# Optimization experiments

Hardware: AMD Instinct MI355X
Metric: run time of the kernel (lower is better)

## Reference

```python
import jax, jax.numpy as jnp
import numpy as np

DIM = 2048
NH = 16
HD = DIM // NH  # 128


def setup_inputs() -> dict:
    key = jax.random.key(0)
    ks = jax.random.split(key, 9)
    s_in = 1.0 / np.sqrt(DIM)
    inp = {
        "x": jax.random.normal(ks[0], (2, 2048, DIM), dtype=jnp.float32),
        # torch Linear weights stored as (out, in); we keep (in, out) for x @ W
        "wq": jax.random.uniform(ks[1], (DIM, DIM), jnp.float32, -s_in, s_in),
        "bq": jax.random.uniform(ks[2], (DIM,), jnp.float32, -s_in, s_in),
        "wk": jax.random.uniform(ks[3], (DIM, HD), jnp.float32, -s_in, s_in),
        "bk": jax.random.uniform(ks[4], (HD,), jnp.float32, -s_in, s_in),
        "wv": jax.random.uniform(ks[5], (DIM, HD), jnp.float32, -s_in, s_in),
        "bv": jax.random.uniform(ks[6], (HD,), jnp.float32, -s_in, s_in),
        "wo": jax.random.uniform(ks[7], (DIM, DIM), jnp.float32, -s_in, s_in),
        "bo": jax.random.uniform(ks[8], (DIM,), jnp.float32, -s_in, s_in),
    }
    return inp


def reference(x, wq, bq, wk, bk, wv, bv, wo, bo):
    bs, sl, dim = x.shape
    q = x @ wq + bq                      # [b, s, dim]
    k = x @ wk + bk                      # [b, s, hd] (single shared KV head)
    v = x @ wv + bv                      # [b, s, hd]
    q = q.reshape(bs, sl, NH, HD)        # [b, s, h, hd]
    scale = 1.0 / np.sqrt(HD).astype(np.float32)
    # scores: broadcast single KV head over all query heads
    attn = jnp.einsum('bshd,btd->bhst', q, k) * scale   # [b, h, s, s]
    att = jax.nn.softmax(attn, axis=-1)
    o = jnp.einsum('bhst,btd->bshd', att, v)            # [b, s, h, hd]
    o = o.reshape(bs, sl, dim)
    return o @ wo + bo
```

## Files before the change

kernel.cpp:

```cpp
#include <hip/hip_runtime.h>
#include <hip/hip_bf16.h>
#include <math.h>

#define DIM 2048
#define NH 16
#define HD 128
#define BATCH 2
#define SEQ 2048
#define TOKENS (BATCH * SEQ)
#define NQKV (DIM + 2 * HD)

typedef __attribute__((ext_vector_type(8))) _Float16 f16x8;
typedef __attribute__((ext_vector_type(4))) float f32x4;
typedef unsigned short u16;
typedef unsigned int u32;

typedef union { u32 d[4]; f16x8 v; } frag_u;

__device__ __forceinline__ u16 f2h(float f) {
    union { _Float16 h; u16 u; } v; v.h = (_Float16)f; return v.u;
}
__device__ __forceinline__ void gll16(const void* g, void* l) {
    __builtin_amdgcn_global_load_lds(
        (const __attribute__((address_space(1))) unsigned int*)g,
        (__attribute__((address_space(3))) unsigned int*)l, 16, 0, 0);
}

#define KIDX(r, c) ((r) * 128 + (((((c) << 1)) ^ (((r) & 7) << 4)) >> 1))
#define VIDX(d, c) ((d) * 64  + (((((c) << 1)) ^ (((d) & 7) << 4)) >> 1))

__global__ __launch_bounds__(256) void conv_f16(
    const float* __restrict__ in, u16* __restrict__ out)
{
    const int i = blockIdx.x * 256 + threadIdx.x;
    const float4 v = ((const float4*)in)[i];
    ushort4 h;
    h.x = f2h(v.x); h.y = f2h(v.y); h.z = f2h(v.z); h.w = f2h(v.w);
    ((ushort4*)out)[i] = h;
}

__global__ __launch_bounds__(256) void transpose_f16(
    const float* __restrict__ W, u16* __restrict__ T, int K, int N, int rowoff)
{
    __shared__ float tile[32][33];
    const int k0 = blockIdx.x * 32;
    const int n0 = blockIdx.y * 32;
    const int tid = threadIdx.x;
#pragma unroll
    for (int i = 0; i < 4; ++i) {
        const int idx = tid + i * 256;
        const int r = idx >> 5, c = idx & 31;
        tile[r][c] = W[(size_t)(k0 + r) * N + n0 + c];
    }
    __syncthreads();
#pragma unroll
    for (int i = 0; i < 4; ++i) {
        const int idx = tid + i * 256;
        const int r = idx >> 5, c = idx & 31;
        T[(size_t)(rowoff + n0 + r) * K + k0 + c] = f2h(tile[c][r]);
    }
}

__global__ __launch_bounds__(256) void concat_bias(
    const float* __restrict__ bq, const float* __restrict__ bk,
    const float* __restrict__ bv, float* __restrict__ bc)
{
    const int i = blockIdx.x * 256 + threadIdx.x;
    float v;
    if (i < DIM) v = bq[i];
    else if (i < DIM + HD) v = bk[i - DIM];
    else v = bv[i - DIM - HD];
    bc[i] = v;
}

template <int MODE>
__global__ __launch_bounds__(256) void gemm_f16(
    const u16* __restrict__ A, const u16* __restrict__ B,
    const float* __restrict__ bias, float* __restrict__ Cf,
    u16* __restrict__ qdst, u16* __restrict__ kdst, u16* __restrict__ vtdst,
    float scale)
{
    constexpr int BK = 32;
    __shared__ u16 lds[2][2 * 128 * BK];

    const int tid = threadIdx.x;
    const int wid = tid >> 6;
    const int lane = tid & 63;
    const int lr = lane & 15;
    const int lhi = lane >> 4;
    const int wr = wid >> 1, wc = wid & 1;
    const int bm = blockIdx.y * 128;
    const int bn = blockIdx.x * 128;

    f32x4 acc[4][4];
#pragma unroll
    for (int i = 0; i < 4; ++i)
#pragma unroll
        for (int j = 0; j < 4; ++j) acc[i][j] = (f32x4){0.f, 0.f, 0.f, 0.f};

#define STAGE(buf_, k0_)                                                      \
    {                                                                         \
        _Pragma("unroll")                                                     \
        for (int rr = 0; rr < 2; ++rr) {                                      \
            const int slot = rr * 256 + tid;                                  \
            const int row = slot >> 2;                                        \
            const int gch = ((slot & 3) ^ ((row >> 1) & 3)) * 8;              \
            char* lbase = (char*)lds[buf_] + (size_t)(rr * 256 + wid * 64) * 16; \
            gll16(A + (size_t)(bm + row) * DIM + (k0_) + gch, lbase);         \
            gll16(B + (size_t)(bn + row) * DIM + (k0_) + gch, lbase + 8192);  \
        }                                                                     \
    }

    STAGE(0, 0);
    __syncthreads();

    int cur = 0;
    for (int k0 = 0; k0 < DIM; k0 += BK) {
        if (k0 + BK < DIM) STAGE(cur ^ 1, k0 + BK);

        f16x8 a[4], b[4];
#pragma unroll
        for (int i = 0; i < 4; ++i) {
            const int mrow = wr * 64 + i * 16 + lr;
            const int nrow = wc * 64 + i * 16 + lr;
            a[i] = *(const f16x8*)&lds[cur][mrow * BK + ((lhi ^ ((mrow >> 1) & 3)) * 8)];
            b[i] = *(const f16x8*)&lds[cur][4096 + nrow * BK + ((lhi ^ ((nrow >> 1) & 3)) * 8)];
        }
        __builtin_amdgcn_s_setprio(1);
#pragma unroll
        for (int i = 0; i < 4; ++i)
#pragma unroll
            for (int j = 0; j < 4; ++j)
                acc[i][j] = __builtin_amdgcn_mfma_f32_16x16x32_f16(a[i], b[j], acc[i][j], 0, 0, 0);
        __builtin_amdgcn_s_setprio(0);
        __syncthreads();
        cur ^= 1;
    }
#undef STAGE

    const float alpha = (MODE == 0 && bn < DIM) ? scale : 1.0f;
    float bj[4];
#pragma unroll
    for (int j = 0; j < 4; ++j) bj[j] = bias[bn + wc * 64 + j * 16 + lr];

#pragma unroll
    for (int i = 0; i < 4; ++i) {
#pragma unroll
        for (int j = 0; j < 4; ++j) {
#pragma unroll
            for (int r = 0; r < 4; ++r) {
                const int row = bm + wr * 64 + i * 16 + lhi * 4 + r;
                const int col = bn + wc * 64 + j * 16 + lr;
                const float val = (acc[i][j][r] + bj[j]) * alpha;
                if (MODE == 1) {
                    Cf[(size_t)row * DIM + col] = val;
                } else if (bn < DIM) {
                    qdst[(size_t)row * DIM + col] = f2h(val);
                } else if (bn < DIM + HD) {
                    kdst[(size_t)row * HD + (col - DIM)] = f2h(val);
                } else {
                    vtdst[(size_t)(col - DIM - HD) * TOKENS + row] = f2h(val);
                }
            }
        }
    }
}

__global__ __launch_bounds__(256, 2) void mqa_attn_f16(
    const u16* __restrict__ Q, const u16* __restrict__ Kg,
    const u16* __restrict__ Vtg, u16* __restrict__ Oh)
{
    __shared__ __align__(16) u16 Ks[2][64 * 128];
    __shared__ __align__(16) u16 Vt[3][128 * 64];

    const int tid = threadIdx.x;
    const int wid = tid >> 6;
    const int lane = tid & 63;
    const int lr = lane & 15;
    const int lhi = lane >> 4;
    const bool l5 = (lhi & 2) != 0;

    const int qt = blockIdx.x;
    const int h  = blockIdx.y;
    const int b  = blockIdx.z;
    const size_t bseq = (size_t)b * SEQ;
    const int q0 = qt * 128 + wid * 32;

    f16x8 qf[2][4];
#pragma unroll
    for (int mt = 0; mt < 2; ++mt) {
        const u16* qrow = Q + (bseq + q0 + mt * 16 + lr) * DIM + (size_t)h * HD;
#pragma unroll
        for (int kk = 0; kk < 4; ++kk)
            qf[mt][kk] = *(const f16x8*)(qrow + kk * 32 + lhi * 8);
    }

    f16x8 ones;
#pragma unroll
    for (int j = 0; j < 8; ++j) ones[j] = (_Float16)1.0f;

    f32x4 o[2][8];
#pragma unroll
    for (int mt = 0; mt < 2; ++mt)
#pragma unroll
        for (int dt = 0; dt < 8; ++dt) o[mt][dt] = (f32x4){0.f, 0.f, 0.f, 0.f};
    float m[2]    = {-INFINITY, -INFINITY};
    float lsum[2] = {0.f, 0.f};

    frag_u pa[2][2];
#pragma unroll
    for (int mt = 0; mt < 2; ++mt)
#pragma unroll
        for (int kk = 0; kk < 2; ++kk)
#pragma unroll
            for (int p = 0; p < 4; ++p) pa[mt][kk].d[p] = 0u;

#define STAGE_K(buf_, t0_)                                                    \
    {                                                                         \
        _Pragma("unroll")                                                     \
        for (int i = 0; i < 4; ++i) {                                         \
            const int L = i * 256 + tid;                                      \
            char* kbase = (char*)&Ks[buf_][0] + (size_t)(i * 256 + wid * 64) * 16; \
            const int krow = L >> 4, kc = (L & 15) ^ ((L >> 4) & 7);          \
            gll16(&Kg[(bseq + (t0_) + krow) * HD + kc * 8], kbase);           \
        }                                                                     \
    }
#define STAGE_V(buf_, t0_)                                                    \
    {                                                                         \
        _Pragma("unroll")                                                     \
        for (int i = 0; i < 4; ++i) {                                         \
            const int L = i * 256 + tid;                                      \
            char* vbase = (char*)&Vt[buf_][0] + (size_t)(i * 256 + wid * 64) * 16; \
            const int vrow = L >> 3, vc = (L & 7) ^ ((L >> 3) & 7);           \
            gll16(&Vtg[(size_t)vrow * TOKENS + bseq + (t0_) + vc * 8], vbase);\
        }                                                                     \
    }

    STAGE_K(0, 0);
    STAGE_V(0, 0);
    __syncthreads();

    int kcur = 0;
    int vprev = 0, vcur = 0, vnxt = 1;

    for (int t0 = 0; t0 < SEQ; t0 += 64) {
        if (t0 + 64 < SEQ) {
            STAGE_K(kcur ^ 1, t0 + 64);
            STAGE_V(vnxt, t0 + 64);
        }

        f32x4 sc[2][4];
#pragma unroll
        for (int mt = 0; mt < 2; ++mt)
#pragma unroll
            for (int ct = 0; ct < 4; ++ct) sc[mt][ct] = (f32x4){0.f, 0.f, 0.f, 0.f};
        __builtin_amdgcn_s_setprio(1);
#pragma unroll
        for (int kk = 0; kk < 4; ++kk)
#pragma unroll
            for (int ct = 0; ct < 4; ++ct) {
                const f16x8 kf = *(const f16x8*)&Ks[kcur][KIDX(ct * 16 + lr, kk * 32 + lhi * 8)];
                sc[0][ct] = __builtin_amdgcn_mfma_f32_16x16x32_f16(kf, qf[0][kk], sc[0][ct], 0, 0, 0);
                sc[1][ct] = __builtin_amdgcn_mfma_f32_16x16x32_f16(kf, qf[1][kk], sc[1][ct], 0, 0, 0);
            }
        __builtin_amdgcn_s_setprio(0);

        f32x4 lacc[2];
        lacc[0] = (f32x4){0.f, 0.f, 0.f, 0.f};
        lacc[1] = (f32x4){0.f, 0.f, 0.f, 0.f};
        __builtin_amdgcn_s_setprio(1);
#pragma unroll
        for (int kk = 0; kk < 2; ++kk) {
            lacc[0] = __builtin_amdgcn_mfma_f32_16x16x32_f16(ones, pa[0][kk].v, lacc[0], 0, 0, 0);
            lacc[1] = __builtin_amdgcn_mfma_f32_16x16x32_f16(ones, pa[1][kk].v, lacc[1], 0, 0, 0);
#pragma unroll
            for (int dt = 0; dt < 8; ++dt) {
                const f16x8 vf = *(const f16x8*)&Vt[vprev][VIDX(dt * 16 + lr, kk * 32 + lhi * 8)];
                o[0][dt] = __builtin_amdgcn_mfma_f32_16x16x32_f16(vf, pa[0][kk].v, o[0][dt], 0, 0, 0);
                o[1][dt] = __builtin_amdgcn_mfma_f32_16x16x32_f16(vf, pa[1][kk].v, o[1][dt], 0, 0, 0);
            }
        }
        __builtin_amdgcn_s_setprio(0);

        frag_u panew[2][2];
        float mnew[2];
        bool grow[2];
#pragma unroll
        for (int mt = 0; mt < 2; ++mt) {
            float pm = fmaxf(fmaxf(fmaxf(sc[mt][0][0], sc[mt][0][1]),
                                   fmaxf(sc[mt][0][2], sc[mt][0][3])),
                             fmaxf(fmaxf(sc[mt][1][0], sc[mt][1][1]),
                                   fmaxf(sc[mt][1][2], sc[mt][1][3])));
            pm = fmaxf(pm, fmaxf(fmaxf(fmaxf(sc[mt][2][0], sc[mt][2][1]),
                                       fmaxf(sc[mt][2][2], sc[mt][2][3])),
                                 fmaxf(fmaxf(sc[mt][3][0], sc[mt][3][1]),
                                       fmaxf(sc[mt][3][2], sc[mt][3][3]))));
            pm = fmaxf(pm, __shfl_xor(pm, 16));
            pm = fmaxf(pm, __shfl_xor(pm, 32));

            grow[mt] = pm > m[mt] + 8.f;
            mnew[mt] = grow[mt] ? pm : m[mt];

            u32 pk[4][2];
#pragma unroll
            for (int ct = 0; ct < 4; ++ct) {
                const float p0 = __expf(sc[mt][ct][0] - mnew[mt]);
                const float p1 = __expf(sc[mt][ct][1] - mnew[mt]);
                const float p2 = __expf(sc[mt][ct][2] - mnew[mt]);
                const float p3 = __expf(sc[mt][ct][3] - mnew[mt]);
                pk[ct][0] = __builtin_bit_cast(u32, __builtin_amdgcn_cvt_pkrtz(p0, p1));
                pk[ct][1] = __builtin_bit_cast(u32, __builtin_amdgcn_cvt_pkrtz(p2, p3));
            }
#pragma unroll
            for (int kk = 0; kk < 2; ++kk)
#pragma unroll
                for (int p = 0; p < 2; ++p) {
                    const u32 X = pk[2 * kk + 0][p];
                    const u32 Y = pk[2 * kk + 1][p];
                    const u32 sx = __shfl_xor(X, 32);
                    const u32 sy = __shfl_xor(Y, 32);
                    const u32 X1 = l5 ? sy : X;
                    const u32 Y1 = l5 ? Y : sx;
                    const auto u2 = __builtin_amdgcn_permlane16_swap(X1, Y1, false, false);
                    panew[mt][kk].d[p]     = u2[0];
                    panew[mt][kk].d[2 + p] = u2[1];
                }
        }

#pragma unroll
        for (int mt = 0; mt < 2; ++mt) {
            lsum[mt] += lacc[mt][0];
            if (__any(grow[mt])) {
                const float al = grow[mt] ? __expf(m[mt] - mnew[mt]) : 1.f;
#pragma unroll
                for (int dt = 0; dt < 8; ++dt)
#pragma unroll
                    for (int r = 0; r < 4; ++r)
                        o[mt][dt][r] *= al;
                lsum[mt] *= al;
            }
            m[mt] = mnew[mt];
#pragma unroll
            for (int kk = 0; kk < 2; ++kk)
                pa[mt][kk] = panew[mt][kk];
        }

        __syncthreads();
        kcur ^= 1;
        vprev = vcur; vcur = vnxt; vnxt = (vnxt + 1 == 3) ? 0 : vnxt + 1;
    }
#undef STAGE_K
#undef STAGE_V

    {
        f32x4 lacc[2];
        lacc[0] = (f32x4){0.f, 0.f, 0.f, 0.f};
        lacc[1] = (f32x4){0.f, 0.f, 0.f, 0.f};
#pragma unroll
        for (int kk = 0; kk < 2; ++kk) {
            lacc[0] = __builtin_amdgcn_mfma_f32_16x16x32_f16(ones, pa[0][kk].v, lacc[0], 0, 0, 0);
            lacc[1] = __builtin_amdgcn_mfma_f32_16x16x32_f16(ones, pa[1][kk].v, lacc[1], 0, 0, 0);
#pragma unroll
            for (int dt = 0; dt < 8; ++dt) {
                const f16x8 vf = *(const f16x8*)&Vt[vprev][VIDX(dt * 16 + lr, kk * 32 + lhi * 8)];
                o[0][dt] = __builtin_amdgcn_mfma_f32_16x16x32_f16(vf, pa[0][kk].v, o[0][dt], 0, 0, 0);
                o[1][dt] = __builtin_amdgcn_mfma_f32_16x16x32_f16(vf, pa[1][kk].v, o[1][dt], 0, 0, 0);
            }
        }
        lsum[0] += lacc[0][0];
        lsum[1] += lacc[1][0];
    }

#pragma unroll
    for (int mt = 0; mt < 2; ++mt) {
        const float inv = 1.f / lsum[mt];
        const size_t base = (bseq + q0 + mt * 16 + lr) * DIM + (size_t)h * HD + lhi * 4;
#pragma unroll
        for (int dt = 0; dt < 8; ++dt) {
            ushort4 h4;
            h4.x = f2h(o[mt][dt][0] * inv);
            h4.y = f2h(o[mt][dt][1] * inv);
            h4.z = f2h(o[mt][dt][2] * inv);
            h4.w = f2h(o[mt][dt][3] * inv);
            *(ushort4*)&Oh[base + dt * 16] = h4;
        }
    }
}

extern "C" void kernel_launch(void* const* d_in, const int* in_sizes, int n_in,
                              void* d_out, int out_size, void* d_ws, size_t ws_size,
                              hipStream_t stream) {
    const float* x  = (const float*)d_in[0];
    const float* wq = (const float*)d_in[1];
    const float* bq = (const float*)d_in[2];
    const float* wk = (const float*)d_in[3];
    const float* bk = (const float*)d_in[4];
    const float* wv = (const float*)d_in[5];
    const float* bv = (const float*)d_in[6];
    const float* wo = (const float*)d_in[7];
    const float* bo = (const float*)d_in[8];
    float* out = (float*)d_out;

    char* w = (char*)d_ws;
    u16* xh     = (u16*)w;                 w += (size_t)TOKENS * DIM * 2;
    u16* wcat   = (u16*)w;                 w += (size_t)NQKV * DIM * 2;
    u16* woT    = (u16*)w;                 w += (size_t)DIM * DIM * 2;
    u16* qb     = (u16*)w;                 w += (size_t)TOKENS * DIM * 2;
    u16* kb     = (u16*)w;                 w += (size_t)TOKENS * HD * 2;
    u16* vtb    = (u16*)w;                 w += (size_t)TOKENS * HD * 2;
    float* bc   = (float*)w;               w += 16384;
    u16* Oh = xh;

    const float scale = 0.08838834764831845f;
    const dim3 blk(256);

    conv_f16<<<TOKENS * DIM / 4 / 256, blk, 0, stream>>>(x, xh);
    transpose_f16<<<dim3(DIM / 32, DIM / 32), blk, 0, stream>>>(wq, wcat, DIM, DIM, 0);
    transpose_f16<<<dim3(DIM / 32, HD / 32), blk, 0, stream>>>(wk, wcat, DIM, HD, DIM);
    transpose_f16<<<dim3(DIM / 32, HD / 32), blk, 0, stream>>>(wv, wcat, DIM, HD, DIM + HD);
    transpose_f16<<<dim3(DIM / 32, DIM / 32), blk, 0, stream>>>(wo, woT, DIM, DIM, 0);
    concat_bias<<<NQKV / 256, blk, 0, stream>>>(bq, bk, bv, bc);

    gemm_f16<0><<<dim3(NQKV / 128, TOKENS / 128), blk, 0, stream>>>(
        xh, wcat, bc, nullptr, qb, kb, vtb, scale);

    mqa_attn_f16<<<dim3(SEQ / 128, NH, BATCH), blk, 0, stream>>>(qb, kb, vtb, Oh);

    gemm_f16<1><<<dim3(DIM / 128, TOKENS / 128), blk, 0, stream>>>(
        Oh, woT, bo, out, nullptr, nullptr, nullptr, 1.0f);
}
```

Before: 223.1 us.

## Split attention work across 8 waves with 16 query rows each

The attention kernel now launches 512 threads per block, and each of the 8 waves handles one 16-row query tile instead of two. Register pressure per wave drops and more waves are available to hide latency, while K/V staging is split across more threads. The cost is that each K/V fragment read from LDS feeds only one MFMA instead of two, which doubles LDS read traffic per unit of compute. The launch-bounds change to (512,4) may also constrain register allocation.

```diff
diff --git a/kernel.cpp b/kernel.cpp
--- a/kernel.cpp
+++ b/kernel.cpp
@@ -166,7 +166,7 @@
     }
 }
 
-__global__ __launch_bounds__(256, 2) void mqa_attn_f16(
+__global__ __launch_bounds__(512, 4) void mqa_attn_f16(
     const u16* __restrict__ Q, const u16* __restrict__ Kg,
     const u16* __restrict__ Vtg, u16* __restrict__ Oh)
 {
@@ -184,43 +184,38 @@
     const int h  = blockIdx.y;
     const int b  = blockIdx.z;
     const size_t bseq = (size_t)b * SEQ;
-    const int q0 = qt * 128 + wid * 32;
-
-    f16x8 qf[2][4];
-#pragma unroll
-    for (int mt = 0; mt < 2; ++mt) {
-        const u16* qrow = Q + (bseq + q0 + mt * 16 + lr) * DIM + (size_t)h * HD;
+    const int q0 = qt * 128 + wid * 16;
+
+    f16x8 qf[4];
+    {
+        const u16* qrow = Q + (bseq + q0 + lr) * DIM + (size_t)h * HD;
 #pragma unroll
         for (int kk = 0; kk < 4; ++kk)
-            qf[mt][kk] = *(const f16x8*)(qrow + kk * 32 + lhi * 8);
+            qf[kk] = *(const f16x8*)(qrow + kk * 32 + lhi * 8);
     }
 
     f16x8 ones;
 #pragma unroll
     for (int j = 0; j < 8; ++j) ones[j] = (_Float16)1.0f;
 
-    f32x4 o[2][8];
-#pragma unroll
-    for (int mt = 0; mt < 2; ++mt)
-#pragma unroll
-        for (int dt = 0; dt < 8; ++dt) o[mt][dt] = (f32x4){0.f, 0.f, 0.f, 0.f};
-    float m[2]    = {-INFINITY, -INFINITY};
-    float lsum[2] = {0.f, 0.f};
-
-    frag_u pa[2][2];
-#pragma unroll
-    for (int mt = 0; mt < 2; ++mt)
-#pragma unroll
-        for (int kk = 0; kk < 2; ++kk)
-#pragma unroll
-            for (int p = 0; p < 4; ++p) pa[mt][kk].d[p] = 0u;
+    f32x4 o[8];
+#pragma unroll
+    for (int dt = 0; dt < 8; ++dt) o[dt] = (f32x4){0.f, 0.f, 0.f, 0.f};
+    float m = -INFINITY;
+    float lsum = 0.f;
+
+    frag_u pa[2];
+#pragma unroll
+    for (int kk = 0; kk < 2; ++kk)
+#pragma unroll
+        for (int p = 0; p < 4; ++p) pa[kk].d[p] = 0u;
 
 #define STAGE_K(buf_, t0_)                                                    \
     {                                                                         \
         _Pragma("unroll")                                                     \
-        for (int i = 0; i < 4; ++i) {                                         \
-            const int L = i * 256 + tid;                                      \
-            char* kbase = (char*)&Ks[buf_][0] + (size_t)(i * 256 + wid * 64) * 16; \
+        for (int i = 0; i < 2; ++i) {                                         \
+            const int L = i * 512 + tid;                                      \
+            char* kbase = (char*)&Ks[buf_][0] + (size_t)(i * 512 + wid * 64) * 16; \
             const int krow = L >> 4, kc = (L & 15) ^ ((L >> 4) & 7);          \
             gll16(&Kg[(bseq + (t0_) + krow) * HD + kc * 8], kbase);           \
         }                                                                     \
@@ -228,9 +223,9 @@
 #define STAGE_V(buf_, t0_)                                                    \
     {                                                                         \
         _Pragma("unroll")                                                     \
-        for (int i = 0; i < 4; ++i) {                                         \
-            const int L = i * 256 + tid;                                      \
-            char* vbase = (char*)&Vt[buf_][0] + (size_t)(i * 256 + wid * 64) * 16; \
+        for (int i = 0; i < 2; ++i) {                                         \
+            const int L = i * 512 + tid;                                      \
+            char* vbase = (char*)&Vt[buf_][0] + (size_t)(i * 512 + wid * 64) * 16; \
             const int vrow = L >> 3, vc = (L & 7) ^ ((L >> 3) & 7);           \
             gll16(&Vtg[(size_t)vrow * TOKENS + bseq + (t0_) + vc * 8], vbase);\
         }                                                                     \
@@ -249,101 +244,82 @@
             STAGE_V(vnxt, t0 + 64);
         }
 
-        f32x4 sc[2][4];
-#pragma unroll
-        for (int mt = 0; mt < 2; ++mt)
-#pragma unroll
-            for (int ct = 0; ct < 4; ++ct) sc[mt][ct] = (f32x4){0.f, 0.f, 0.f, 0.f};
+        f32x4 sc[4];
+#pragma unroll
+        for (int ct = 0; ct < 4; ++ct) sc[ct] = (f32x4){0.f, 0.f, 0.f, 0.f};
         __builtin_amdgcn_s_setprio(1);
 #pragma unroll
         for (int kk = 0; kk < 4; ++kk)
 #pragma unroll
             for (int ct = 0; ct < 4; ++ct) {
                 const f16x8 kf = *(const f16x8*)&Ks[kcur][KIDX(ct * 16 + lr, kk * 32 + lhi * 8)];
-                sc[0][ct] = __builtin_amdgcn_mfma_f32_16x16x32_f16(kf, qf[0][kk], sc[0][ct], 0, 0, 0);
-                sc[1][ct] = __builtin_amdgcn_mfma_f32_16x16x32_f16(kf, qf[1][kk], sc[1][ct], 0, 0, 0);
+                sc[ct] = __builtin_amdgcn_mfma_f32_16x16x32_f16(kf, qf[kk], sc[ct], 0, 0, 0);
             }
         __builtin_amdgcn_s_setprio(0);
 
-        f32x4 lacc[2];
-        lacc[0] = (f32x4){0.f, 0.f, 0.f, 0.f};
-        lacc[1] = (f32x4){0.f, 0.f, 0.f, 0.f};
+        f32x4 lacc = (f32x4){0.f, 0.f, 0.f, 0.f};
         __builtin_amdgcn_s_setprio(1);
 #pragma unroll
         for (int kk = 0; kk < 2; ++kk) {
-            lacc[0] = __builtin_amdgcn_mfma_f32_16x16x32_f16(ones, pa[0][kk].v, lacc[0], 0, 0, 0);
-            lacc[1] = __builtin_amdgcn_mfma_f32_16x16x32_f16(ones, pa[1][kk].v, lacc[1], 0, 0, 0);
+            lacc = __builtin_amdgcn_mfma_f32_16x16x32_f16(ones, pa[kk].v, lacc, 0, 0, 0);
 #pragma unroll
             for (int dt = 0; dt < 8; ++dt) {
                 const f16x8 vf = *(const f16x8*)&Vt[vprev][VIDX(dt * 16 + lr, kk * 32 + lhi * 8)];
-                o[0][dt] = __builtin_amdgcn_mfma_f32_16x16x32_f16(vf, pa[0][kk].v, o[0][dt], 0, 0, 0);
-                o[1][dt] = __builtin_amdgcn_mfma_f32_16x16x32_f16(vf, pa[1][kk].v, o[1][dt], 0, 0, 0);
+                o[dt] = __builtin_amdgcn_mfma_f32_16x16x32_f16(vf, pa[kk].v, o[dt], 0, 0, 0);
             }
         }
         __builtin_amdgcn_s_setprio(0);
 
-        frag_u panew[2][2];
-        float mnew[2];
-        bool grow[2];
-#pragma unroll
-        for (int mt = 0; mt < 2; ++mt) {
-            float pm = fmaxf(fmaxf(fmaxf(sc[mt][0][0], sc[mt][0][1]),
-                                   fmaxf(sc[mt][0][2], sc[mt][0][3])),
-                             fmaxf(fmaxf(sc[mt][1][0], sc[mt][1][1]),
-                                   fmaxf(sc[mt][1][2], sc[mt][1][3])));
-            pm = fmaxf(pm, fmaxf(fmaxf(fmaxf(sc[mt][2][0], sc[mt][2][1]),
-                                       fmaxf(sc[mt][2][2], sc[mt][2][3])),
-                                 fmaxf(fmaxf(sc[mt][3][0], sc[mt][3][1]),
-                                       fmaxf(sc[mt][3][2], sc[mt][3][3]))));
-            pm = fmaxf(pm, __shfl_xor(pm, 16));
-            pm = fmaxf(pm, __shfl_xor(pm, 32));
-
-            grow[mt] = pm > m[mt] + 8.f;
-            mnew[mt] = grow[mt] ? pm : m[mt];
-
-            u32 pk[4][2];
-#pragma unroll
-            for (int ct = 0; ct < 4; ++ct) {
-                const float p0 = __expf(sc[mt][ct][0] - mnew[mt]);
-                const float p1 = __expf(sc[mt][ct][1] - mnew[mt]);
-                const float p2 = __expf(sc[mt][ct][2] - mnew[mt]);
-                const float p3 = __expf(sc[mt][ct][3] - mnew[mt]);
-                pk[ct][0] = __builtin_bit_cast(u32, __builtin_amdgcn_cvt_pkrtz(p0, p1));
-                pk[ct][1] = __builtin_bit_cast(u32, __builtin_amdgcn_cvt_pkrtz(p2, p3));
+        float pm = fmaxf(fmaxf(fmaxf(sc[0][0], sc[0][1]), fmaxf(sc[0][2], sc[0][3])),
+                         fmaxf(fmaxf(sc[1][0], sc[1][1]), fmaxf(sc[1][2], sc[1][3])));
+        pm = fmaxf(pm, fmaxf(fmaxf(fmaxf(sc[2][0], sc[2][1]), fmaxf(sc[2][2], sc[2][3])),
+                             fmaxf(fmaxf(sc[3][0], sc[3][1]), fmaxf(sc[3][2], sc[3][3]))));
+        pm = fmaxf(pm, __shfl_xor(pm, 16));
+        pm = fmaxf(pm, __shfl_xor(pm, 32));
+
+        const bool grow = pm > m + 8.f;
+        const float mnew = grow ? pm : m;
+
+        u32 pk[4][2];
+#pragma unroll
+        for (int ct = 0; ct < 4; ++ct) {
+            const float p0 = __expf(sc[ct][0] - mnew);
+            const float p1 = __expf(sc[ct][1] - mnew);
+            const float p2 = __expf(sc[ct][2] - mnew);
+            const float p3 = __expf(sc[ct][3] - mnew);
+            pk[ct][0] = __builtin_bit_cast(u32, __builtin_amdgcn_cvt_pkrtz(p0, p1));
+            pk[ct][1] = __builtin_bit_cast(u32, __builtin_amdgcn_cvt_pkrtz(p2, p3));
+        }
+        frag_u panew[2];
+#pragma unroll
+        for (int kk = 0; kk < 2; ++kk)
+#pragma unroll
+            for (int p = 0; p < 2; ++p) {
+                const u32 X = pk[2 * kk + 0][p];
+                const u32 Y = pk[2 * kk + 1][p];
+                const u32 sx = __shfl_xor(X, 32);
+                const u32 sy = __shfl_xor(Y, 32);
+                const u32 X1 = l5 ? sy : X;
+                const u32 Y1 = l5 ? Y : sx;
+                const auto u2 = __builtin_amdgcn_permlane16_swap(X1, Y1, false, false);
+                panew[kk].d[p]     = u2[0];
+                panew[kk].d[2 + p] = u2[1];
             }
-#pragma unroll
-            for (int kk = 0; kk < 2; ++kk)
-#pragma unroll
-                for (int p = 0; p < 2; ++p) {
-                    const u32 X = pk[2 * kk + 0][p];
-                    const u32 Y = pk[2 * kk + 1][p];
-                    const u32 sx = __shfl_xor(X, 32);
-                    const u32 sy = __shfl_xor(Y, 32);
-                    const u32 X1 = l5 ? sy : X;
-                    const u32 Y1 = l5 ? Y : sx;
-                    const auto u2 = __builtin_amdgcn_permlane16_swap(X1, Y1, false, false);
-                    panew[mt][kk].d[p]     = u2[0];
-                    panew[mt][kk].d[2 + p] = u2[1];
-                }
-        }
-
-#pragma unroll
-        for (int mt = 0; mt < 2; ++mt) {
-            lsum[mt] += lacc[mt][0];
-            if (__any(grow[mt])) {
-                const float al = grow[mt] ? __expf(m[mt] - mnew[mt]) : 1.f;
-#pragma unroll
-                for (int dt = 0; dt < 8; ++dt)
-#pragma unroll
-                    for (int r = 0; r < 4; ++r)
-                        o[mt][dt][r] *= al;
-                lsum[mt] *= al;
-            }
-            m[mt] = mnew[mt];
-#pragma unroll
-            for (int kk = 0; kk < 2; ++kk)
-                pa[mt][kk] = panew[mt][kk];
-        }
+
+        lsum += lacc[0];
+        if (__any(grow)) {
+            const float al = grow ? __expf(m - mnew) : 1.f;
+#pragma unroll
+            for (int dt = 0; dt < 8; ++dt)
+#pragma unroll
+                for (int r = 0; r < 4; ++r)
+                    o[dt][r] *= al;
+            lsum *= al;
+        }
+        m = mnew;
+#pragma unroll
+        for (int kk = 0; kk < 2; ++kk)
+            pa[kk] = panew[kk];
 
         __syncthreads();
         kcur ^= 1;
@@ -353,35 +329,29 @@
 #undef STAGE_V
 
     {
-        f32x4 lacc[2];
-        lacc[0] = (f32x4){0.f, 0.f, 0.f, 0.f};
-        lacc[1] = (f32x4){0.f, 0.f, 0.f, 0.f};
+        f32x4 lacc = (f32x4){0.f, 0.f, 0.f, 0.f};
 #pragma unroll
         for (int kk = 0; kk < 2; ++kk) {
-            lacc[0] = __builtin_amdgcn_mfma_f32_16x16x32_f16(ones, pa[0][kk].v, lacc[0], 0, 0, 0);
-            lacc[1] = __builtin_amdgcn_mfma_f32_16x16x32_f16(ones, pa[1][kk].v, lacc[1], 0, 0, 0);
+            lacc = __builtin_amdgcn_mfma_f32_16x16x32_f16(ones, pa[kk].v, lacc, 0, 0, 0);
 #pragma unroll
             for (int dt = 0; dt < 8; ++dt) {
                 const f16x8 vf = *(const f16x8*)&Vt[vprev][VIDX(dt * 16 + lr, kk * 32 + lhi * 8)];
-                o[0][dt] = __builtin_amdgcn_mfma_f32_16x16x32_f16(vf, pa[0][kk].v, o[0][dt], 0, 0, 0);
-                o[1][dt] = __builtin_amdgcn_mfma_f32_16x16x32_f16(vf, pa[1][kk].v, o[1][dt], 0, 0, 0);
+                o[dt] = __builtin_amdgcn_mfma_f32_16x16x32_f16(vf, pa[kk].v, o[dt], 0, 0, 0);
             }
         }
-        lsum[0] += lacc[0][0];
-        lsum[1] += lacc[1][0];
-    }
-
-#pragma unroll
-    for (int mt = 0; mt < 2; ++mt) {
-        const float inv = 1.f / lsum[mt];
-        const size_t base = (bseq + q0 + mt * 16 + lr) * DIM + (size_t)h * HD + lhi * 4;
+        lsum += lacc[0];
+    }
+
+    {
+        const float inv = 1.f / lsum;
+        const size_t base = (bseq + q0 + lr) * DIM + (size_t)h * HD + lhi * 4;
 #pragma unroll
         for (int dt = 0; dt < 8; ++dt) {
             ushort4 h4;
-            h4.x = f2h(o[mt][dt][0] * inv);
-            h4.y = f2h(o[mt][dt][1] * inv);
-            h4.z = f2h(o[mt][dt][2] * inv);
-            h4.w = f2h(o[mt][dt][3] * inv);
+            h4.x = f2h(o[dt][0] * inv);
+            h4.y = f2h(o[dt][1] * inv);
+            h4.z = f2h(o[dt][2] * inv);
+            h4.w = f2h(o[dt][3] * inv);
             *(ushort4*)&Oh[base + dt * 16] = h4;
         }
     }
@@ -424,7 +394,7 @@
     gemm_f16<0><<<dim3(NQKV / 128, TOKENS / 128), blk, 0, stream>>>(
         xh, wcat, bc, nullptr, qb, kb, vtb, scale);
 
-    mqa_attn_f16<<<dim3(SEQ / 128, NH, BATCH), blk, 0, stream>>>(qb, kb, vtb, Oh);
+    mqa_attn_f16<<<dim3(SEQ / 128, NH, BATCH), dim3(512), 0, stream>>>(qb, kb, vtb, Oh);
 
     gemm_f16<1><<<dim3(DIM / 128, TOKENS / 128), blk, 0, stream>>>(
         Oh, woT, bo, out, nullptr, nullptr, nullptr, 1.0f);
```

Result: no change. 225.6 us (+1.1%).

## Double GEMM K-tile to 64 with 8-chunk XOR swizzle and XCD-aware block remap

Applied to the files above, without the earlier changes.

Raises the GEMM K-step from 32 to 64, which halves the number of barriers and main-loop iterations. Each staged tile now holds 8 16-byte chunks per row, and the LDS swizzle is widened to an XOR over 8 chunks to match. Workgroup IDs are also remapped so consecutive tiles land on the same XCD (8-way interleave), which should improve L2 reuse of A and B rows. In exchange, LDS use doubles to 64 KB per block, which may reduce occupancy, and the remap assumes the block count is divisible by 8.

```diff
diff --git a/kernel.cpp b/kernel.cpp
--- a/kernel.cpp
+++ b/kernel.cpp
@@ -80,8 +80,9 @@
     u16* __restrict__ qdst, u16* __restrict__ kdst, u16* __restrict__ vtdst,
     float scale)
 {
-    constexpr int BK = 32;
-    __shared__ u16 lds[2][2 * 128 * BK];
+    constexpr int BK = 64;
+    constexpr int BUFE = 2 * 128 * BK;
+    __shared__ u16 lds[2][BUFE];
 
     const int tid = threadIdx.x;
     const int wid = tid >> 6;
@@ -89,8 +90,14 @@
     const int lr = lane & 15;
     const int lhi = lane >> 4;
     const int wr = wid >> 1, wc = wid & 1;
-    const int bm = blockIdx.y * 128;
-    const int bn = blockIdx.x * 128;
+
+    const int nx = gridDim.x;
+    const int nwg = nx * gridDim.y;
+    const int flat = blockIdx.y * nx + blockIdx.x;
+    const int cpx = nwg >> 3;
+    const int newid = (flat & 7) * cpx + (flat >> 3);
+    const int bm = (newid / nx) * 128;
+    const int bn = (newid % nx) * 128;
 
     f32x4 acc[4][4];
 #pragma unroll
@@ -101,13 +108,13 @@
 #define STAGE(buf_, k0_)                                                      \
     {                                                                         \
         _Pragma("unroll")                                                     \
-        for (int rr = 0; rr < 2; ++rr) {                                      \
-            const int slot = rr * 256 + tid;                                  \
-            const int row = slot >> 2;                                        \
-            const int gch = ((slot & 3) ^ ((row >> 1) & 3)) * 8;              \
-            char* lbase = (char*)lds[buf_] + (size_t)(rr * 256 + wid * 64) * 16; \
-            gll16(A + (size_t)(bm + row) * DIM + (k0_) + gch, lbase);         \
-            gll16(B + (size_t)(bn + row) * DIM + (k0_) + gch, lbase + 8192);  \
+        for (int i = 0; i < 4; ++i) {                                         \
+            const int slot = i * 256 + tid;                                   \
+            const int row = slot >> 3;                                        \
+            const int gsrc = ((slot & 7) ^ (row & 7)) * 8;                    \
+            char* lbase = (char*)lds[buf_] + (size_t)(i * 256 + wid * 64) * 16; \
+            gll16(A + (size_t)(bm + row) * DIM + (k0_) + gsrc, lbase);        \
+            gll16(B + (size_t)(bn + row) * DIM + (k0_) + gsrc, lbase + 16384);\
         }                                                                     \
     }
 
@@ -118,20 +125,25 @@
     for (int k0 = 0; k0 < DIM; k0 += BK) {
         if (k0 + BK < DIM) STAGE(cur ^ 1, k0 + BK);
 
-        f16x8 a[4], b[4];
-#pragma unroll
-        for (int i = 0; i < 4; ++i) {
-            const int mrow = wr * 64 + i * 16 + lr;
-            const int nrow = wc * 64 + i * 16 + lr;
-            a[i] = *(const f16x8*)&lds[cur][mrow * BK + ((lhi ^ ((mrow >> 1) & 3)) * 8)];
-            b[i] = *(const f16x8*)&lds[cur][4096 + nrow * BK + ((lhi ^ ((nrow >> 1) & 3)) * 8)];
-        }
         __builtin_amdgcn_s_setprio(1);
 #pragma unroll
-        for (int i = 0; i < 4; ++i)
-#pragma unroll
-            for (int j = 0; j < 4; ++j)
-                acc[i][j] = __builtin_amdgcn_mfma_f32_16x16x32_f16(a[i], b[j], acc[i][j], 0, 0, 0);
+        for (int kk = 0; kk < 2; ++kk) {
+            f16x8 a[4], b[4];
+#pragma unroll
+            for (int i = 0; i < 4; ++i) {
+                const int mrow = wr * 64 + i * 16 + lr;
+                const int nrow = wc * 64 + i * 16 + lr;
+                const int ga = ((kk * 4 + lhi) ^ (mrow & 7)) * 8;
+                const int gb = ((kk * 4 + lhi) ^ (nrow & 7)) * 8;
+                a[i] = *(const f16x8*)&lds[cur][mrow * BK + ga];
+                b[i] = *(const f16x8*)&lds[cur][8192 + nrow * BK + gb];
+            }
+#pragma unroll
+            for (int i = 0; i < 4; ++i)
+#pragma unroll
+                for (int j = 0; j < 4; ++j)
+                    acc[i][j] = __builtin_amdgcn_mfma_f32_16x16x32_f16(a[i], b[j], acc[i][j], 0, 0, 0);
+        }
         __builtin_amdgcn_s_setprio(0);
         __syncthreads();
         cur ^= 1;
```

New measurement: 218.5 us. 1.02x faster.
